# Performance work log

Measured on AMD Instinct MI355X. Metric: run time of the kernel, lower is better.

The kernel has to match this reference:

```python
import jax, jax.numpy as jnp
import numpy as np

N_HEAD = 16
D_MODEL = 1024
D_HEAD = 64
B = 2
S = 2048      # query length
M = 512       # memory length
K = S + M     # key length
L = 2 * K - 1 # relative position table length
SCALE = 1.0 / np.sqrt(D_MODEL)  # NOTE: module scales by 1/sqrt(d_model), not d_head
EPS = 1e-5


def layer_norm(x, gamma, beta):
    mu = jnp.mean(x, axis=-1, keepdims=True)
    var = jnp.mean(jnp.square(x - mu), axis=-1, keepdims=True)
    return (x - mu) * jax.lax.rsqrt(var + EPS) * gamma + beta


def skew(qpos, mem_len):
    # qpos: (B, H, S, 2K-1) -> relative-position scores aligned to keys (B, H, S, K)
    b, h, s, l = qpos.shape
    k_len = (l + 1) // 2
    pad = jnp.full((b, h, s, 1), -jnp.inf, dtype=qpos.dtype)
    rel = jnp.concatenate([qpos, pad], axis=-1)          # (B,H,S,2K)
    rel = rel.reshape(b, h, s * (l + 1))[..., : s * l]    # drop tail, shift rows
    rel = rel.reshape(b, h, s, l)
    start = (k_len - 1) - mem_len
    return rel[..., start : start + k_len]


def setup_inputs() -> dict:
    key = jax.random.key(0)
    ks = jax.random.split(key, 8)
    w_scale = 1.0 / np.sqrt(D_MODEL)
    hidden = jax.random.normal(ks[0], (B, S, D_MODEL), jnp.float32)
    memory = jax.random.normal(ks[1], (B, M, D_MODEL), jnp.float32)
    pos_emb = jax.random.normal(ks[2], (B, L, D_HEAD), jnp.float32)
    Wq = jax.random.normal(ks[3], (D_MODEL, N_HEAD * D_HEAD), jnp.float32) * w_scale
    Wk = jax.random.normal(ks[4], (D_MODEL, N_HEAD * D_HEAD), jnp.float32) * w_scale
    Wv = jax.random.normal(ks[5], (D_MODEL, N_HEAD * D_HEAD), jnp.float32) * w_scale
    Wo = jax.random.normal(ks[6], (N_HEAD * D_HEAD, D_MODEL), jnp.float32) * w_scale
    gamma = jnp.ones((D_MODEL,), jnp.float32)
    beta = jnp.zeros((D_MODEL,), jnp.float32)
    # causal mask with memory: query i may attend keys j <= i + M; True = drop
    i = jnp.arange(S)[:, None]
    j = jnp.arange(K)[None, :]
    mask = j > (i + M)  # (S, K) bool
    return {"hidden": hidden, "pos_emb": pos_emb, "memory": memory,
            "Wq": Wq, "Wk": Wk, "Wv": Wv, "Wo": Wo,
            "gamma": gamma, "beta": beta, "mask": mask}


def reference(hidden, pos_emb, memory, Wq, Wk, Wv, Wo, gamma, beta, mask):
    combined = jnp.concatenate([memory, hidden], axis=1)  # (B, K, D)
    hn = layer_norm(hidden, gamma, beta)                  # pre_lnorm
    cn = layer_norm(combined, gamma, beta)
    q = (hn @ Wq).reshape(B, S, N_HEAD, D_HEAD).transpose(0, 2, 1, 3)  # (B,H,S,Dh)
    k = (cn @ Wk).reshape(B, K, N_HEAD, D_HEAD).transpose(0, 2, 1, 3)  # (B,H,K,Dh)
    v = (cn @ Wv).reshape(B, K, N_HEAD, D_HEAD).transpose(0, 2, 1, 3)  # (B,H,K,Dh)
    scores = jnp.einsum("bhsd,bhkd->bhsk", q, k)           # content term
    qpos = jnp.einsum("bhsd,bld->bhsl", q, pos_emb)        # position term (B,H,S,2K-1)
    scores = (scores + skew(qpos, M)) * SCALE
    scores = jnp.where(mask[None, None], -jnp.inf, scores)
    attn = jax.nn.softmax(scores, axis=-1)
    atten_vec = jnp.einsum("bhsk,bhkd->bshd", attn, v).reshape(B, S, N_HEAD * D_HEAD)
    output = atten_vec @ Wo
    # faithful quirk: residual uses the layer-normed hidden when pre_lnorm=True
    return hn + output
```

## Files before the change

### kernel.cpp

```cpp
#include <hip/hip_runtime.h>

typedef unsigned short u16;
typedef float f32x4 __attribute__((ext_vector_type(4)));
typedef short short8 __attribute__((ext_vector_type(8)));

#define MFMA_BF16(a, b, c) __builtin_amdgcn_mfma_f32_16x16x32_bf16((a), (b), (c), 0, 0, 0)

#define NEG_BIG (-30000.0f)

typedef __attribute__((address_space(1))) const void gas_void;
typedef __attribute__((address_space(3))) void las_void;

__device__ __forceinline__ float bf2f(u16 v) {
  union { unsigned int u; float f; } c; c.u = ((unsigned int)v) << 16; return c.f;
}
__device__ __forceinline__ u16 f2bf(float f) {
  union { float f; unsigned int u; } c; c.f = f;
  return (u16)((c.u + 0x7fffu + ((c.u >> 16) & 1u)) >> 16);
}

__global__ __launch_bounds__(256) void cast_pe_k(const float* __restrict__ src, u16* __restrict__ dst,
                                                 int n4, int* __restrict__ ctr) {
  const int idx = blockIdx.x * 256 + threadIdx.x;
  if (idx == 0) *ctr = 0;
  if (idx >= n4) return;
  const float4 d = *(const float4*)&src[idx * 4];
  ushort4 o;
  o.x = f2bf(d.x); o.y = f2bf(d.y); o.z = f2bf(d.z); o.w = f2bf(d.w);
  *(ushort4*)&dst[idx * 4] = o;
}

__global__ __launch_bounds__(256) void transpose_k(const float* __restrict__ W0, const float* __restrict__ W1,
                                                   const float* __restrict__ W2, const float* __restrict__ W3,
                                                   u16* __restrict__ Wt) {
  __shared__ float t[32][33];
  const float* W = (blockIdx.z == 0) ? W0 : (blockIdx.z == 1) ? W1 : (blockIdx.z == 2) ? W2 : W3;
  u16* dst = Wt + (size_t)blockIdx.z * 1024 * 1024;
  const int tx = threadIdx.x, ty = threadIdx.y;
  const int x0 = blockIdx.x * 32, y0 = blockIdx.y * 32;
#pragma unroll
  for (int i = 0; i < 32; i += 8)
    t[ty + i][tx] = W[(size_t)(y0 + ty + i) * 1024 + x0 + tx];
  __syncthreads();
#pragma unroll
  for (int i = 0; i < 32; i += 8)
    dst[(size_t)(x0 + ty + i) * 1024 + y0 + tx] = f2bf(t[tx][ty + i]);
}

__global__ __launch_bounds__(256) void ln_k(const float* __restrict__ hid, const float* __restrict__ mem,
                                            const float* __restrict__ gam, const float* __restrict__ bet,
                                            u16* __restrict__ cn) {
  const int row = blockIdx.x;
  const int b = (row >= 2560) ? 1 : 0;
  const int r = row - b * 2560;
  const float* src = (r < 512) ? (mem + ((size_t)b * 512 + r) * 1024)
                               : (hid + ((size_t)b * 2048 + (r - 512)) * 1024);
  const int tid = threadIdx.x;
  const float4 d = *(const float4*)&src[tid * 4];
  float x[4] = {d.x, d.y, d.z, d.w};
  float s = x[0] + x[1] + x[2] + x[3];
  float q = x[0]*x[0] + x[1]*x[1] + x[2]*x[2] + x[3]*x[3];
#pragma unroll
  for (int o = 1; o < 64; o <<= 1) { s += __shfl_xor(s, o); q += __shfl_xor(q, o); }
  __shared__ float sb[4], qsb[4];
  const int wave = tid >> 6;
  if ((tid & 63) == 0) { sb[wave] = s; qsb[wave] = q; }
  __syncthreads();
  s = sb[0] + sb[1] + sb[2] + sb[3];
  q = qsb[0] + qsb[1] + qsb[2] + qsb[3];
  const float mu = s * (1.0f / 1024.0f);
  const float var = q * (1.0f / 1024.0f) - mu * mu;
  const float rstd = rsqrtf(fmaxf(var, 0.0f) + 1e-5f);
  u16 o4[4];
#pragma unroll
  for (int i = 0; i < 4; ++i) {
    const int c = tid * 4 + i;
    o4[i] = f2bf((x[i] - mu) * rstd * gam[c] + bet[c]);
  }
  uint2 pk;
  pk.x = (unsigned)o4[0] | ((unsigned)o4[1] << 16);
  pk.y = (unsigned)o4[2] | ((unsigned)o4[3] << 16);
  *(uint2*)&cn[((size_t)b * 2560 + r) * 1024 + tid * 4] = pk;
}

__global__ __launch_bounds__(256, 3) void gemm128_k(const u16* __restrict__ A, const u16* __restrict__ Bt,
                                                    u16* __restrict__ qb, u16* __restrict__ kbo,
                                                    u16* __restrict__ vtb) {
  __shared__ u16 smem[16384];
  const int tid = threadIdx.x;
  const int lane = tid & 63, w = tid >> 6;
  const int quad = lane >> 4, l15 = lane & 15, r7 = l15 & 7;
  const int wr = w >> 1, wc = w & 1;
  const int row0 = blockIdx.y * 128, col0 = blockIdx.x * 128;
  const int rloc = w * 8 + (lane >> 3);
  const int cg = ((lane & 7) ^ ((lane >> 3) & 7)) * 8;
  const u16* ga = A + (size_t)(row0 + rloc) * 1024 + cg;
  const u16* gb = Bt + (size_t)(col0 + rloc) * 1024 + cg;
  f32x4 z = {0.f, 0.f, 0.f, 0.f};
  f32x4 acc[4][4];
#pragma unroll
  for (int m = 0; m < 4; ++m)
#pragma unroll
    for (int n = 0; n < 4; ++n) acc[m][n] = z;
  for (int kt = 0; kt < 16; ++kt) {
    const int k0 = kt * 64;
#pragma unroll
    for (int g2 = 0; g2 < 4; ++g2) {
      __builtin_amdgcn_global_load_lds((gas_void*)(ga + (size_t)g2 * 32 * 1024 + k0),
                                       (las_void*)(smem + (g2 * 32 + w * 8) * 64), 16, 0, 0);
      __builtin_amdgcn_global_load_lds((gas_void*)(gb + (size_t)g2 * 32 * 1024 + k0),
                                       (las_void*)(smem + 8192 + (g2 * 32 + w * 8) * 64), 16, 0, 0);
    }
    __syncthreads();
    short8 af0[4], af1[4];
#pragma unroll
    for (int m = 0; m < 4; ++m) {
      const int row = wr * 64 + m * 16 + l15;
      af0[m] = *(const short8*)&smem[row * 64 + (quad ^ r7) * 8];
      af1[m] = *(const short8*)&smem[row * 64 + ((quad + 4) ^ r7) * 8];
    }
#pragma unroll
    for (int n = 0; n < 4; ++n) {
      const int row = wc * 64 + n * 16 + l15;
      const short8 bf0 = *(const short8*)&smem[8192 + row * 64 + (quad ^ r7) * 8];
      const short8 bf1 = *(const short8*)&smem[8192 + row * 64 + ((quad + 4) ^ r7) * 8];
#pragma unroll
      for (int m = 0; m < 4; ++m) {
        acc[m][n] = MFMA_BF16(af0[m], bf0, acc[m][n]);
        acc[m][n] = MFMA_BF16(af1[m], bf1, acc[m][n]);
      }
    }
    __syncthreads();
  }
  const int nc = col0 >> 10;
  if (nc != 2) {
#pragma unroll
    for (int m = 0; m < 4; ++m) {
#pragma unroll
      for (int n = 0; n < 4; ++n) {
#pragma unroll
        for (int r = 0; r < 4; ++r) {
          const int R = row0 + wr * 64 + m * 16 + quad * 4 + r;
          const int C = col0 + wc * 64 + n * 16 + l15;
          const float v = acc[m][n][r];
          const int c = C & 1023, h = c >> 6, dh = c & 63;
          const int b = (R >= 2560) ? 1 : 0, kk = R - b * 2560;
          if (nc == 0) {
            if (kk >= 512)
              qb[(((size_t)(b * 16 + h)) * 2048 + (kk - 512)) * 64 + dh] = f2bf(v * 0.03125f);
          } else {
            kbo[(((size_t)(b * 16 + h)) * 2560 + kk) * 64 + dh] = f2bf(v);
          }
        }
      }
    }
  } else {
#pragma unroll
    for (int m = 0; m < 4; ++m)
#pragma unroll
      for (int n = 0; n < 4; ++n)
#pragma unroll
        for (int r = 0; r < 4; ++r) {
          const int rl = wr * 64 + m * 16 + quad * 4 + r;
          const int cl = wc * 64 + n * 16 + l15;
          smem[cl * 128 + (rl ^ ((cl & 7) << 3))] = f2bf(acc[m][n][r]);
        }
    __syncthreads();
    const int bb = (row0 >= 2560) ? 1 : 0;
    const int kk0 = row0 - bb * 2560;
#pragma unroll
    for (int half = 0; half < 2; ++half) {
      const int cl = (tid >> 2) + half * 64;
      const int c = (col0 - 2048) + cl;
      const int hh = c >> 6, dh = c & 63;
      u16* dst = &vtb[(((size_t)(bb * 16 + hh)) * 64 + dh) * 2560 + kk0];
#pragma unroll
      for (int inner = 0; inner < 4; ++inner) {
        const int rl = inner * 32 + (tid & 3) * 8;
        *(short8*)(dst + rl) = *(const short8*)&smem[cl * 128 + (rl ^ ((cl & 7) << 3))];
      }
    }
  }
}

__global__ __launch_bounds__(256) void gemm_out_k(const u16* __restrict__ A, const u16* __restrict__ Bt,
                                                  float* __restrict__ outf,
                                                  const u16* __restrict__ resid) {
  __shared__ u16 As[2][64][40];
  __shared__ u16 Bs[2][64][40];
  const int tid = threadIdx.x;
  const int lane = tid & 63, wave = tid >> 6;
  const int quad = lane >> 4, l15 = lane & 15;
  const int row0 = blockIdx.y * 64, col0 = blockIdx.x * 64;
  const int sr = tid >> 2, sc8 = (tid & 3) * 8;
  const u16* ga = A + (size_t)(row0 + sr) * 1024 + sc8;
  const u16* gb = Bt + (size_t)(col0 + sr) * 1024 + sc8;
  f32x4 z = {0.f, 0.f, 0.f, 0.f};
  f32x4 acc[4];
#pragma unroll
  for (int i = 0; i < 4; ++i) acc[i] = z;
  *(uint4*)&As[0][sr][sc8] = *(const uint4*)ga;
  *(uint4*)&Bs[0][sr][sc8] = *(const uint4*)gb;
  __syncthreads();
  for (int it = 0; it < 32; ++it) {
    const int cur = it & 1;
    const int kn = (it + 1 < 32) ? (it + 1) * 32 : it * 32;
    const uint4 ua = *(const uint4*)(ga + kn);
    const uint4 ub = *(const uint4*)(gb + kn);
    const short8 af = *(const short8*)&As[cur][16 * wave + l15][quad * 8];
#pragma unroll
    for (int n = 0; n < 4; ++n)
      acc[n] = MFMA_BF16(af, *(const short8*)&Bs[cur][16 * n + l15][quad * 8], acc[n]);
    *(uint4*)&As[cur ^ 1][sr][sc8] = ua;
    *(uint4*)&Bs[cur ^ 1][sr][sc8] = ub;
    __syncthreads();
  }
#pragma unroll
  for (int n = 0; n < 4; ++n) {
#pragma unroll
    for (int r = 0; r < 4; ++r) {
      const int R = row0 + 16 * wave + quad * 4 + r;
      const int C = col0 + 16 * n + l15;
      const size_t rrow = (size_t)(R >> 11) * 2560 + 512 + (R & 2047);
      outf[(size_t)R * 1024 + C] = acc[n][r] + bf2f(resid[rrow * 1024 + C]);
    }
  }
}

__global__ __launch_bounds__(512, 4) void attn_k(const u16* __restrict__ q, const u16* __restrict__ kb,
                                                 const u16* __restrict__ vt, const u16* __restrict__ pe,
                                                 u16* __restrict__ p0, u16* __restrict__ p1,
                                                 float* __restrict__ l0, float* __restrict__ l1,
                                                 int* __restrict__ ctr) {
  __shared__ u16 Kt[2][64][72];
  __shared__ u16 Vt[2][64][72];
  __shared__ u16 Pw[8][16][68];
  volatile int* mailbox = (volatile int*)&Pw[0][0][64];
  const int tid = threadIdx.x, lane = tid & 63, wave = tid >> 6;
  const int quad = lane >> 4, l15 = lane & 15;
  const int sr = tid >> 3, sc8 = (tid & 7) * 8;
  const f32x4 z = {0.f, 0.f, 0.f, 0.f};
  for (;;) {
    if (tid == 0) *mailbox = atomicAdd(ctr, 1);
    __syncthreads();
    const int item = *mailbox;
    if (item >= 1024) return;
    const int qt = 15 - (item >> 6);
    const int bh = (item & 63) >> 1, half = item & 1;
    const int b = bh >> 4, h = bh & 15;
    const int qi0 = qt * 128 + wave * 16;
    const int nh = qt + 5;
    const int t0 = half * nh, t1 = t0 + nh;
    const u16* qrow = q + ((size_t)bh * 2048 + qi0 + l15) * 64 + quad * 8;
    const short8 aq0 = *(const short8*)qrow;
    const short8 aq1 = *(const short8*)(qrow + 32);
    const u16* pp = pe + ((long)b * 5119 - qi0 + 2032 + l15) * 64 + quad * 8 + (size_t)t0 * 4096;
    f32x4 acc[4];
#pragma unroll
    for (int i = 0; i < 4; ++i) acc[i] = z;
    float lrow[4] = {0.f, 0.f, 0.f, 0.f};
    const int jlast = qi0 + 527;
    *(uint4*)&Kt[0][sr][sc8] = *(const uint4*)&kb[((size_t)bh * 2560 + t0 * 64 + sr) * 64 + sc8];
    *(uint4*)&Vt[0][sr][sc8] = *(const uint4*)&vt[((size_t)bh * 64 + sr) * 2560 + t0 * 64 + sc8];
    __syncthreads();
    for (int jt = t0; jt < t1; ++jt) {
      const int j0 = jt * 64;
      const int cur = (jt - t0) & 1;
      const int jn = (jt + 1 < t1) ? (jt + 1) : jt;
      const uint4 ku = *(const uint4*)&kb[((size_t)bh * 2560 + jn * 64 + sr) * 64 + sc8];
      const uint4 vu = *(const uint4*)&vt[((size_t)bh * 64 + sr) * 2560 + jn * 64 + sc8];
      if (j0 <= jlast) {
        short8 pb[5], pb2[5];
#pragma unroll
        for (int g = 0; g < 5; ++g) {
          pb[g]  = *(const short8*)(pp + 1024 * g);
          pb2[g] = *(const short8*)(pp + 1024 * g + 32);
        }
        f32x4 sc[4];
#pragma unroll
        for (int s = 0; s < 4; ++s) {
          sc[s] = MFMA_BF16(aq0, *(const short8*)&Kt[cur][16 * s + l15][quad * 8], z);
          sc[s] = MFMA_BF16(aq1, *(const short8*)&Kt[cur][16 * s + l15][32 + quad * 8], sc[s]);
        }
        f32x4 qp[5];
#pragma unroll
        for (int g = 0; g < 5; ++g) {
          qp[g] = MFMA_BF16(aq0, pb[g], z);
          qp[g] = MFMA_BF16(aq1, pb2[g], qp[g]);
        }
#pragma unroll
        for (int r = 0; r < 4; ++r) {
          const int di = quad * 4 + r;
          const int o = l15 - di + 15;
          const int src = quad * 16 + (o & 15);
          const float g0 = __shfl(qp[0][r], src);
          const float g1 = __shfl(qp[1][r], src);
          const float g2 = __shfl(qp[2][r], src);
          const float g3 = __shfl(qp[3][r], src);
          const float g4 = __shfl(qp[4][r], src);
          const bool lo = (o < 16);
          float s0 = sc[0][r] + (lo ? g0 : g1);
          float s1 = sc[1][r] + (lo ? g1 : g2);
          float s2 = sc[2][r] + (lo ? g2 : g3);
          float s3 = sc[3][r] + (lo ? g3 : g4);
          const int jlim = qi0 + di + 512 - j0 - l15;
          if (0 > jlim)  s0 = NEG_BIG;
          if (16 > jlim) s1 = NEG_BIG;
          if (32 > jlim) s2 = NEG_BIG;
          if (48 > jlim) s3 = NEG_BIG;
          const float p0v = __expf(s0);
          const float p1v = __expf(s1);
          const float p2v = __expf(s2);
          const float p3v = __expf(s3);
          lrow[r] += (p0v + p1v) + (p2v + p3v);
          Pw[wave][di][l15]      = f2bf(p0v);
          Pw[wave][di][16 + l15] = f2bf(p1v);
          Pw[wave][di][32 + l15] = f2bf(p2v);
          Pw[wave][di][48 + l15] = f2bf(p3v);
        }
        asm volatile("s_waitcnt lgkmcnt(0)" ::: "memory");
        const short8 pf0 = *(const short8*)&Pw[wave][l15][quad * 8];
        const short8 pf1 = *(const short8*)&Pw[wave][l15][32 + quad * 8];
#pragma unroll
        for (int n = 0; n < 4; ++n) {
          acc[n] = MFMA_BF16(pf0, *(const short8*)&Vt[cur][16 * n + l15][quad * 8], acc[n]);
          acc[n] = MFMA_BF16(pf1, *(const short8*)&Vt[cur][16 * n + l15][32 + quad * 8], acc[n]);
        }
      }
      *(uint4*)&Kt[cur ^ 1][sr][sc8] = ku;
      *(uint4*)&Vt[cur ^ 1][sr][sc8] = vu;
      __syncthreads();
      pp += 4096;
    }
    u16* od = half ? p1 : p0;
    float* ol = half ? l1 : l0;
#pragma unroll
    for (int r = 0; r < 4; ++r) {
      float lsum = lrow[r];
#pragma unroll
      for (int o = 1; o < 16; o <<= 1) lsum += __shfl_xor(lsum, o);
      const int s = qi0 + quad * 4 + r;
      if (l15 == 0) ol[(size_t)bh * 2048 + s] = lsum;
#pragma unroll
      for (int n = 0; n < 4; ++n) {
        const int c = h * 64 + n * 16 + l15;
        od[((size_t)b * 2048 + s) * 1024 + c] = f2bf(acc[n][r]);
      }
    }
  }
}

__global__ __launch_bounds__(256) void combine_k(u16* __restrict__ av, const u16* __restrict__ p1,
                                                 const float* __restrict__ l0, const float* __restrict__ l1) {
  const int idx = blockIdx.x * 256 + threadIdx.x;
  const int base = idx * 4;
  const int row = base >> 10;
  const int col = base & 1023;
  const int b = row >> 11, s = row & 2047;
  const int h = col >> 6;
  const size_t li = ((size_t)(b * 16 + h)) * 2048 + s;
  const float inv = 1.0f / (l0[li] + l1[li]);
  const ushort4 a0 = *(const ushort4*)&av[(size_t)base];
  const ushort4 a1 = *(const ushort4*)&p1[(size_t)base];
  ushort4 o;
  o.x = f2bf((bf2f(a0.x) + bf2f(a1.x)) * inv);
  o.y = f2bf((bf2f(a0.y) + bf2f(a1.y)) * inv);
  o.z = f2bf((bf2f(a0.z) + bf2f(a1.z)) * inv);
  o.w = f2bf((bf2f(a0.w) + bf2f(a1.w)) * inv);
  *(ushort4*)&av[(size_t)base] = o;
}

extern "C" void kernel_launch(void* const* d_in, const int* in_sizes, int n_in,
                              void* d_out, int out_size, void* d_ws, size_t ws_size,
                              hipStream_t stream) {
  const float* hidden = (const float*)d_in[0];
  const float* pe     = (const float*)d_in[1];
  const float* memv   = (const float*)d_in[2];
  const float* Wq     = (const float*)d_in[3];
  const float* Wk     = (const float*)d_in[4];
  const float* Wv     = (const float*)d_in[5];
  const float* Wo     = (const float*)d_in[6];
  const float* gam    = (const float*)d_in[7];
  const float* bet    = (const float*)d_in[8];

  u16* ws  = (u16*)d_ws;
  u16* cn  = ws;
  u16* qb  = cn  + (size_t)5120 * 1024;
  u16* kb  = qb  + (size_t)4096 * 1024;
  u16* vt  = kb  + (size_t)5120 * 1024;
  u16* av  = vt  + (size_t)5120 * 1024;
  u16* wt  = av  + (size_t)4096 * 1024;
  u16* peb = wt  + (size_t)4 * 1024 * 1024;
  u16* p1  = peb + (size_t)2 * 5119 * 64;
  float* l0 = (float*)(p1 + (size_t)4096 * 1024);
  float* l1 = l0 + (size_t)32 * 2048;
  int* ctr  = (int*)(l1 + (size_t)32 * 2048);

  const int pe_n4 = (2 * 5119 * 64) / 4;
  cast_pe_k<<<(pe_n4 + 255) / 256, 256, 0, stream>>>(pe, peb, pe_n4, ctr);
  ln_k<<<5120, 256, 0, stream>>>(hidden, memv, gam, bet, cn);
  transpose_k<<<dim3(32, 32, 4), dim3(32, 8), 0, stream>>>(Wq, Wk, Wv, Wo, wt);
  gemm128_k<<<dim3(24, 40), 256, 0, stream>>>(cn, wt, qb, kb, vt);
  attn_k<<<768, 512, 0, stream>>>(qb, kb, vt, peb, av, p1, l0, l1, ctr);
  combine_k<<<4096, 256, 0, stream>>>(av, p1, l0, l1);
  gemm_out_k<<<dim3(16, 64), 256, 0, stream>>>(av, wt + (size_t)3 * 1024 * 1024,
                                               (float*)d_out, cn);
}
```

Before: 331.8 us.

## Use direct global-to-LDS loads with XOR swizzle in attention and output GEMM

The output projection GEMM moves from 64x64 tiles with K-step 32 to 128x128 tiles with K-step 64. It fills LDS with global_load_lds direct copies into an XOR-swizzled, unpadded layout, and each wave now computes a 4x4 block of MFMA tiles. The attention kernel also replaces its register-staged K/V prefetch with direct global-to-LDS loads and swizzled LDS reads, which frees registers and removes the padding. In exchange, the output GEMM drops double buffering: it loads, syncs and computes with no overlap. It also launches fewer blocks, so the GPU is less fully occupied.

```diff
diff --git a/kernel.cpp b/kernel.cpp
--- a/kernel.cpp
+++ b/kernel.cpp
@@ -183,46 +183,66 @@
   }
 }
 
-__global__ __launch_bounds__(256) void gemm_out_k(const u16* __restrict__ A, const u16* __restrict__ Bt,
-                                                  float* __restrict__ outf,
-                                                  const u16* __restrict__ resid) {
-  __shared__ u16 As[2][64][40];
-  __shared__ u16 Bs[2][64][40];
+__global__ __launch_bounds__(256, 3) void gemm_out_k(const u16* __restrict__ A, const u16* __restrict__ Bt,
+                                                     float* __restrict__ outf,
+                                                     const u16* __restrict__ resid) {
+  __shared__ u16 smem[16384];
   const int tid = threadIdx.x;
-  const int lane = tid & 63, wave = tid >> 6;
-  const int quad = lane >> 4, l15 = lane & 15;
-  const int row0 = blockIdx.y * 64, col0 = blockIdx.x * 64;
-  const int sr = tid >> 2, sc8 = (tid & 3) * 8;
-  const u16* ga = A + (size_t)(row0 + sr) * 1024 + sc8;
-  const u16* gb = Bt + (size_t)(col0 + sr) * 1024 + sc8;
+  const int lane = tid & 63, w = tid >> 6;
+  const int quad = lane >> 4, l15 = lane & 15, r7 = l15 & 7;
+  const int wr = w >> 1, wc = w & 1;
+  const int row0 = blockIdx.y * 128, col0 = blockIdx.x * 128;
+  const int rloc = w * 8 + (lane >> 3);
+  const int cg = ((lane & 7) ^ ((lane >> 3) & 7)) * 8;
+  const u16* ga = A + (size_t)(row0 + rloc) * 1024 + cg;
+  const u16* gb = Bt + (size_t)(col0 + rloc) * 1024 + cg;
   f32x4 z = {0.f, 0.f, 0.f, 0.f};
-  f32x4 acc[4];
-#pragma unroll
-  for (int i = 0; i < 4; ++i) acc[i] = z;
-  *(uint4*)&As[0][sr][sc8] = *(const uint4*)ga;
-  *(uint4*)&Bs[0][sr][sc8] = *(const uint4*)gb;
-  __syncthreads();
-  for (int it = 0; it < 32; ++it) {
-    const int cur = it & 1;
-    const int kn = (it + 1 < 32) ? (it + 1) * 32 : it * 32;
-    const uint4 ua = *(const uint4*)(ga + kn);
-    const uint4 ub = *(const uint4*)(gb + kn);
-    const short8 af = *(const short8*)&As[cur][16 * wave + l15][quad * 8];
-#pragma unroll
-    for (int n = 0; n < 4; ++n)
-      acc[n] = MFMA_BF16(af, *(const short8*)&Bs[cur][16 * n + l15][quad * 8], acc[n]);
-    *(uint4*)&As[cur ^ 1][sr][sc8] = ua;
-    *(uint4*)&Bs[cur ^ 1][sr][sc8] = ub;
-    __syncthreads();
-  }
-#pragma unroll
-  for (int n = 0; n < 4; ++n) {
-#pragma unroll
-    for (int r = 0; r < 4; ++r) {
-      const int R = row0 + 16 * wave + quad * 4 + r;
-      const int C = col0 + 16 * n + l15;
-      const size_t rrow = (size_t)(R >> 11) * 2560 + 512 + (R & 2047);
-      outf[(size_t)R * 1024 + C] = acc[n][r] + bf2f(resid[rrow * 1024 + C]);
+  f32x4 acc[4][4];
+#pragma unroll
+  for (int m = 0; m < 4; ++m)
+#pragma unroll
+    for (int n = 0; n < 4; ++n) acc[m][n] = z;
+  for (int kt = 0; kt < 16; ++kt) {
+    const int k0 = kt * 64;
+#pragma unroll
+    for (int g2 = 0; g2 < 4; ++g2) {
+      __builtin_amdgcn_global_load_lds((gas_void*)(ga + (size_t)g2 * 32 * 1024 + k0),
+                                       (las_void*)(smem + (g2 * 32 + w * 8) * 64), 16, 0, 0);
+      __builtin_amdgcn_global_load_lds((gas_void*)(gb + (size_t)g2 * 32 * 1024 + k0),
+                                       (las_void*)(smem + 8192 + (g2 * 32 + w * 8) * 64), 16, 0, 0);
+    }
+    __syncthreads();
+    short8 af0[4], af1[4];
+#pragma unroll
+    for (int m = 0; m < 4; ++m) {
+      const int row = wr * 64 + m * 16 + l15;
+      af0[m] = *(const short8*)&smem[row * 64 + (quad ^ r7) * 8];
+      af1[m] = *(const short8*)&smem[row * 64 + ((quad + 4) ^ r7) * 8];
+    }
+#pragma unroll
+    for (int n = 0; n < 4; ++n) {
+      const int row = wc * 64 + n * 16 + l15;
+      const short8 bf0 = *(const short8*)&smem[8192 + row * 64 + (quad ^ r7) * 8];
+      const short8 bf1 = *(const short8*)&smem[8192 + row * 64 + ((quad + 4) ^ r7) * 8];
+#pragma unroll
+      for (int m = 0; m < 4; ++m) {
+        acc[m][n] = MFMA_BF16(af0[m], bf0, acc[m][n]);
+        acc[m][n] = MFMA_BF16(af1[m], bf1, acc[m][n]);
+      }
+    }
+    __syncthreads();
+  }
+#pragma unroll
+  for (int m = 0; m < 4; ++m) {
+#pragma unroll
+    for (int n = 0; n < 4; ++n) {
+#pragma unroll
+      for (int r = 0; r < 4; ++r) {
+        const int R = row0 + wr * 64 + m * 16 + quad * 4 + r;
+        const int C = col0 + wc * 64 + n * 16 + l15;
+        const size_t rrow = (size_t)(R >> 11) * 2560 + 512 + (R & 2047);
+        outf[(size_t)R * 1024 + C] = acc[m][n][r] + bf2f(resid[rrow * 1024 + C]);
+      }
     }
   }
 }
@@ -232,13 +252,14 @@
                                                  u16* __restrict__ p0, u16* __restrict__ p1,
                                                  float* __restrict__ l0, float* __restrict__ l1,
                                                  int* __restrict__ ctr) {
-  __shared__ u16 Kt[2][64][72];
-  __shared__ u16 Vt[2][64][72];
+  __shared__ u16 Kt[2][64][64];
+  __shared__ u16 Vt[2][64][64];
   __shared__ u16 Pw[8][16][68];
   volatile int* mailbox = (volatile int*)&Pw[0][0][64];
   const int tid = threadIdx.x, lane = tid & 63, wave = tid >> 6;
-  const int quad = lane >> 4, l15 = lane & 15;
-  const int sr = tid >> 3, sc8 = (tid & 7) * 8;
+  const int quad = lane >> 4, l15 = lane & 15, r7 = l15 & 7;
+  const int srow = wave * 8 + (lane >> 3);
+  const int sch8 = ((lane & 7) ^ ((lane >> 3) & 7)) * 8;
   const f32x4 z = {0.f, 0.f, 0.f, 0.f};
   for (;;) {
     if (tid == 0) *mailbox = atomicAdd(ctr, 1);
@@ -254,21 +275,27 @@
     const u16* qrow = q + ((size_t)bh * 2048 + qi0 + l15) * 64 + quad * 8;
     const short8 aq0 = *(const short8*)qrow;
     const short8 aq1 = *(const short8*)(qrow + 32);
+    const u16* kp = kb + ((size_t)bh * 2560 + srow) * 64 + sch8;
+    const u16* vp = vt + ((size_t)bh * 64 + srow) * 2560 + sch8;
     const u16* pp = pe + ((long)b * 5119 - qi0 + 2032 + l15) * 64 + quad * 8 + (size_t)t0 * 4096;
     f32x4 acc[4];
 #pragma unroll
     for (int i = 0; i < 4; ++i) acc[i] = z;
     float lrow[4] = {0.f, 0.f, 0.f, 0.f};
     const int jlast = qi0 + 527;
-    *(uint4*)&Kt[0][sr][sc8] = *(const uint4*)&kb[((size_t)bh * 2560 + t0 * 64 + sr) * 64 + sc8];
-    *(uint4*)&Vt[0][sr][sc8] = *(const uint4*)&vt[((size_t)bh * 64 + sr) * 2560 + t0 * 64 + sc8];
+    __builtin_amdgcn_global_load_lds((gas_void*)(kp + (size_t)t0 * 4096),
+                                     (las_void*)(&Kt[0][wave * 8][0]), 16, 0, 0);
+    __builtin_amdgcn_global_load_lds((gas_void*)(vp + t0 * 64),
+                                     (las_void*)(&Vt[0][wave * 8][0]), 16, 0, 0);
     __syncthreads();
     for (int jt = t0; jt < t1; ++jt) {
       const int j0 = jt * 64;
       const int cur = (jt - t0) & 1;
       const int jn = (jt + 1 < t1) ? (jt + 1) : jt;
-      const uint4 ku = *(const uint4*)&kb[((size_t)bh * 2560 + jn * 64 + sr) * 64 + sc8];
-      const uint4 vu = *(const uint4*)&vt[((size_t)bh * 64 + sr) * 2560 + jn * 64 + sc8];
+      __builtin_amdgcn_global_load_lds((gas_void*)(kp + (size_t)jn * 4096),
+                                       (las_void*)(&Kt[cur ^ 1][wave * 8][0]), 16, 0, 0);
+      __builtin_amdgcn_global_load_lds((gas_void*)(vp + jn * 64),
+                                       (las_void*)(&Vt[cur ^ 1][wave * 8][0]), 16, 0, 0);
       if (j0 <= jlast) {
         short8 pb[5], pb2[5];
 #pragma unroll
@@ -279,8 +306,8 @@
         f32x4 sc[4];
 #pragma unroll
         for (int s = 0; s < 4; ++s) {
-          sc[s] = MFMA_BF16(aq0, *(const short8*)&Kt[cur][16 * s + l15][quad * 8], z);
-          sc[s] = MFMA_BF16(aq1, *(const short8*)&Kt[cur][16 * s + l15][32 + quad * 8], sc[s]);
+          sc[s] = MFMA_BF16(aq0, *(const short8*)&Kt[cur][16 * s + l15][(quad ^ r7) * 8], z);
+          sc[s] = MFMA_BF16(aq1, *(const short8*)&Kt[cur][16 * s + l15][((quad + 4) ^ r7) * 8], sc[s]);
         }
         f32x4 qp[5];
 #pragma unroll
@@ -323,12 +350,10 @@
         const short8 pf1 = *(const short8*)&Pw[wave][l15][32 + quad * 8];
 #pragma unroll
         for (int n = 0; n < 4; ++n) {
-          acc[n] = MFMA_BF16(pf0, *(const short8*)&Vt[cur][16 * n + l15][quad * 8], acc[n]);
-          acc[n] = MFMA_BF16(pf1, *(const short8*)&Vt[cur][16 * n + l15][32 + quad * 8], acc[n]);
-        }
-      }
-      *(uint4*)&Kt[cur ^ 1][sr][sc8] = ku;
-      *(uint4*)&Vt[cur ^ 1][sr][sc8] = vu;
+          acc[n] = MFMA_BF16(pf0, *(const short8*)&Vt[cur][16 * n + l15][(quad ^ r7) * 8], acc[n]);
+          acc[n] = MFMA_BF16(pf1, *(const short8*)&Vt[cur][16 * n + l15][((quad + 4) ^ r7) * 8], acc[n]);
+        }
+      }
       __syncthreads();
       pp += 4096;
     }
@@ -403,6 +428,6 @@
   gemm128_k<<<dim3(24, 40), 256, 0, stream>>>(cn, wt, qb, kb, vt);
   attn_k<<<768, 512, 0, stream>>>(qb, kb, vt, peb, av, p1, l0, l1, ctr);
   combine_k<<<4096, 256, 0, stream>>>(av, p1, l0, l1);
-  gemm_out_k<<<dim3(16, 64), 256, 0, stream>>>(av, wt + (size_t)3 * 1024 * 1024,
-                                               (float*)d_out, cn);
-}
+  gemm_out_k<<<dim3(8, 32), 256, 0, stream>>>(av, wt + (size_t)3 * 1024 * 1024,
+                                              (float*)d_out, cn);
+}
```

Measured after the change: 313.5 us (median of 2 runs). -5.5%, faster.
